# Kernel optimization log

Measured on AMD Instinct MI355X. Metric: run time of the kernel, lower is better.

The kernel has to match this reference:

```python
import jax, jax.numpy as jnp
import numpy as np

B, T_ENC, D = 64, 512, 256
MEL, R = 80, 5
T_DEC = 200
IN = MEL * R  # 400


def _p(key, shape, scale):
    return jax.random.normal(key, shape, dtype=jnp.float32) * scale


def setup_inputs() -> dict:
    key = jax.random.key(0)
    ks = jax.random.split(key, 32)
    s = lambda fan: 1.0 / np.sqrt(fan)
    inp = {
        "enc_out": jax.random.normal(ks[0], (B, T_ENC, D), dtype=jnp.float32),
        "mel_in": jax.random.normal(ks[1], (B, T_DEC, IN), dtype=jnp.float32),
        # prenet: 400 -> 256 -> 128
        "prenet_w1": _p(ks[2], (IN, 256), s(IN)), "prenet_b1": jnp.zeros((256,), jnp.float32),
        "prenet_w2": _p(ks[3], (256, 128), s(256)), "prenet_b2": jnp.zeros((128,), jnp.float32),
        # attention GRUCell: input 128+256=384, hidden 256 (torch gate order r,z,n)
        "att_w_ih": _p(ks[4], (384, 768), s(384)), "att_w_hh": _p(ks[5], (256, 768), s(256)),
        "att_b_ih": jnp.zeros((768,), jnp.float32), "att_b_hh": jnp.zeros((768,), jnp.float32),
        # Bahdanau attention
        "mem_w": _p(ks[6], (D, 256), s(D)),
        "query_w": _p(ks[7], (256, 256), s(256)),
        "att_v": _p(ks[8], (256,), s(256)),
        # project_to_decoder_in: 512 -> 256
        "proj_w": _p(ks[9], (512, 256), s(512)), "proj_b": jnp.zeros((256,), jnp.float32),
        # 2 decoder GRUCells 256->256
        "dec1_w_ih": _p(ks[10], (256, 768), s(256)), "dec1_w_hh": _p(ks[11], (256, 768), s(256)),
        "dec1_b_ih": jnp.zeros((768,), jnp.float32), "dec1_b_hh": jnp.zeros((768,), jnp.float32),
        "dec2_w_ih": _p(ks[12], (256, 768), s(256)), "dec2_w_hh": _p(ks[13], (256, 768), s(256)),
        "dec2_b_ih": jnp.zeros((768,), jnp.float32), "dec2_b_hh": jnp.zeros((768,), jnp.float32),
        # proj_to_mel: 256 -> 400
        "mel_w": _p(ks[14], (256, IN), s(256)), "mel_b": jnp.zeros((IN,), jnp.float32),
    }
    return inp


def _gru(x, h, w_ih, w_hh, b_ih, b_hh):
    gi = x @ w_ih + b_ih
    gh = h @ w_hh + b_hh
    i_r, i_z, i_n = jnp.split(gi, 3, axis=-1)
    h_r, h_z, h_n = jnp.split(gh, 3, axis=-1)
    r = jax.nn.sigmoid(i_r + h_r)
    z = jax.nn.sigmoid(i_z + h_z)
    n = jnp.tanh(i_n + r * h_n)
    return (1.0 - z) * n + z * h


def reference(enc_out, mel_in, prenet_w1, prenet_b1, prenet_w2, prenet_b2,
              att_w_ih, att_w_hh, att_b_ih, att_b_hh, mem_w, query_w, att_v,
              proj_w, proj_b, dec1_w_ih, dec1_w_hh, dec1_b_ih, dec1_b_hh,
              dec2_w_ih, dec2_w_hh, dec2_b_ih, dec2_b_hh, mel_w, mel_b):
    b = enc_out.shape[0]
    # teacher forcing: go frame (zeros) then shifted mel targets
    dec_inputs = jnp.concatenate([jnp.zeros_like(mel_in[:, :1]), mel_in[:, :-1]], axis=1)  # [B,T,400]
    # prenet can be computed for all steps at once (input-only, state-free)
    x = jax.nn.relu(dec_inputs @ prenet_w1 + prenet_b1)
    x = jax.nn.relu(x @ prenet_w2 + prenet_b2)         # [B,T,128]
    xs = jnp.swapaxes(x, 0, 1)                          # [T,B,128]
    proc_mem = enc_out @ mem_w                          # [B,T_enc,256]
    zero = jnp.zeros((b, 256), enc_out.dtype)
    init = (zero, zero, zero, zero)  # att_hidden, context, dec_h1, dec_h2

    def step(carry, xt):
        att_h, ctx, h1, h2 = carry
        att_in = jnp.concatenate([xt, ctx], axis=-1)                 # [B,384]
        att_h = _gru(att_in, att_h, att_w_ih, att_w_hh, att_b_ih, att_b_hh)
        q = att_h @ query_w                                          # [B,256]
        e = jnp.tanh(proc_mem + q[:, None, :]) @ att_v               # [B,T_enc]
        a = jax.nn.softmax(e, axis=-1)
        ctx = jnp.einsum('bt,btd->bd', a, enc_out)                   # [B,256]
        d = jnp.concatenate([att_h, ctx], axis=-1) @ proj_w + proj_b # [B,256]
        h1 = _gru(d, h1, dec1_w_ih, dec1_w_hh, dec1_b_ih, dec1_b_hh)
        d = h1 + d
        h2 = _gru(d, h2, dec2_w_ih, dec2_w_hh, dec2_b_ih, dec2_b_hh)
        d = h2 + d
        out = d @ mel_w + mel_b                                      # [B,400]
        return (att_h, ctx, h1, h2), (out, a)

    _, (outs, aligns) = jax.lax.scan(step, init, xs)
    return jnp.swapaxes(outs, 0, 1), jnp.swapaxes(aligns, 0, 1)
```

## Files before the change

kernel.cpp:

```cpp
#include <hip/hip_runtime.h>
#include <hip/hip_bf16.h>

#define BB   64
#define TT   200
#define TE   512
#define DD   256
#define HH   256
#define GG   768
#define INW  400
#define PN1  256
#define PN2  128

__device__ __forceinline__ float bf2f(unsigned short u) {
    return __uint_as_float(((unsigned)u) << 16);
}
__device__ __forceinline__ float fast_tanh(float x) {
    x = fminf(fmaxf(x, -15.f), 15.f);
    float e = __expf(2.f * x);
    return __fdividef(e - 1.f, e + 1.f);
}
__device__ __forceinline__ float sigm(float x) {
    return __fdividef(1.f, 1.f + __expf(-x));
}

#define FMA4(acc, w4, x0, x1, x2, x3) \
    acc = fmaf(x0, w4.x, acc); acc = fmaf(x1, w4.y, acc); \
    acc = fmaf(x2, w4.z, acc); acc = fmaf(x3, w4.w, acc)

template<int AMODE, int SMODE, bool RELU, bool BIAS>
__global__ __launch_bounds__(256) void gemm_k(
    const float* __restrict__ A, const float* __restrict__ Bm,
    const float* __restrict__ bias, void* __restrict__ Cp,
    int M, int N, int K, int lda, int ldb)
{
    __shared__ __align__(16) float As[16][68];
    __shared__ __align__(16) float Bs[16][68];
    int tid = threadIdx.x;
    int m0 = blockIdx.y * 64, n0 = blockIdx.x * 64;
    int tx = tid & 15, ty = tid >> 4;
    float acc[4][4] = {};
    for (int k0 = 0; k0 < K; k0 += 16) {
        {
            int row = tid >> 2, kq = tid & 3;
            int gr = m0 + row;
            float4 a4;
            if (AMODE == 0) {
                a4 = *(const float4*)(A + (size_t)gr * lda + k0 + kq * 4);
            } else {
                int bb = gr / TT, t = gr % TT;
                if (t == 0) a4 = make_float4(0.f, 0.f, 0.f, 0.f);
                else a4 = *(const float4*)(A + ((size_t)bb * TT + (t - 1)) * INW + k0 + kq * 4);
            }
            As[kq * 4 + 0][row] = a4.x; As[kq * 4 + 1][row] = a4.y;
            As[kq * 4 + 2][row] = a4.z; As[kq * 4 + 3][row] = a4.w;
            int kk = tid >> 4, nq = tid & 15;
            int gc = n0 + nq * 4;
            float4 b4;
            if (gc + 3 < N) {
                b4 = *(const float4*)(Bm + (size_t)(k0 + kk) * ldb + gc);
            } else {
                b4.x = (gc + 0 < N) ? Bm[(size_t)(k0 + kk) * ldb + gc + 0] : 0.f;
                b4.y = (gc + 1 < N) ? Bm[(size_t)(k0 + kk) * ldb + gc + 1] : 0.f;
                b4.z = (gc + 2 < N) ? Bm[(size_t)(k0 + kk) * ldb + gc + 2] : 0.f;
                b4.w = (gc + 3 < N) ? Bm[(size_t)(k0 + kk) * ldb + gc + 3] : 0.f;
            }
            *(float4*)&Bs[kk][nq * 4] = b4;
        }
        __syncthreads();
#pragma unroll
        for (int kk = 0; kk < 16; ++kk) {
            float4 av = *(const float4*)&As[kk][ty * 4];
            float4 bv = *(const float4*)&Bs[kk][tx * 4];
            acc[0][0] = fmaf(av.x, bv.x, acc[0][0]); acc[0][1] = fmaf(av.x, bv.y, acc[0][1]);
            acc[0][2] = fmaf(av.x, bv.z, acc[0][2]); acc[0][3] = fmaf(av.x, bv.w, acc[0][3]);
            acc[1][0] = fmaf(av.y, bv.x, acc[1][0]); acc[1][1] = fmaf(av.y, bv.y, acc[1][1]);
            acc[1][2] = fmaf(av.y, bv.z, acc[1][2]); acc[1][3] = fmaf(av.y, bv.w, acc[1][3]);
            acc[2][0] = fmaf(av.z, bv.x, acc[2][0]); acc[2][1] = fmaf(av.z, bv.y, acc[2][1]);
            acc[2][2] = fmaf(av.z, bv.z, acc[2][2]); acc[2][3] = fmaf(av.z, bv.w, acc[2][3]);
            acc[3][0] = fmaf(av.w, bv.x, acc[3][0]); acc[3][1] = fmaf(av.w, bv.y, acc[3][1]);
            acc[3][2] = fmaf(av.w, bv.z, acc[3][2]); acc[3][3] = fmaf(av.w, bv.w, acc[3][3]);
        }
        __syncthreads();
    }
#pragma unroll
    for (int i = 0; i < 4; ++i) {
#pragma unroll
        for (int j = 0; j < 4; ++j) {
            int r = m0 + ty * 4 + i, c = n0 + tx * 4 + j;
            if (c >= N) continue;
            float v = acc[i][j];
            if (BIAS) v += bias[c];
            if (RELU) v = fmaxf(v, 0.f);
            if (SMODE == 0) ((float*)Cp)[(size_t)r * N + c] = v;
            else if (SMODE == 1) ((float*)Cp)[((size_t)(r % TT) * GG + c) * 64 + (r / TT)] = v;
            else if (SMODE == 2) ((__hip_bfloat16*)Cp)[(size_t)r * N + c] = __float2bfloat16(v);
            else ((float*)Cp)[(size_t)c * M + r] = v;
        }
    }
}

template<bool BF16>
__global__ __launch_bounds__(256) void trans_k(const float* __restrict__ in, int IR, int IC,
                                               int rowoff, void* __restrict__ out)
{
    int idx = blockIdx.x * 256 + threadIdx.x;
    if (idx >= IR * IC) return;
    int c = idx / IR, r = idx % IR;
    float v = in[(size_t)(r + rowoff) * IC + c];
    if (BF16) ((__hip_bfloat16*)out)[idx] = __float2bfloat16(v);
    else ((float*)out)[idx] = v;
}

__global__ __launch_bounds__(256) void tobf16_k(const float* __restrict__ in,
                                                __hip_bfloat16* __restrict__ out, size_t n)
{
    for (size_t i = (size_t)blockIdx.x * 256 + threadIdx.x; i < n; i += (size_t)gridDim.x * 256)
        out[i] = __float2bfloat16(in[i]);
}

__global__ __launch_bounds__(256) void bfuse_k(const float* __restrict__ bih,
                                               const float* __restrict__ projb,
                                               const float* __restrict__ W, int N,
                                               float* __restrict__ out)
{
    int c = blockIdx.x * 256 + threadIdx.x;
    if (c >= N) return;
    float s = bih[c];
    for (int j = 0; j < 256; ++j) s = fmaf(projb[j], W[(size_t)j * N + c], s);
    out[c] = s;
}

__global__ __launch_bounds__(256) void s1_attgru(
    const float* __restrict__ xgi_t, const float* __restrict__ ctxT,
    const float* __restrict__ hT, float* __restrict__ hTn,
    const float* __restrict__ WihcT, const float* __restrict__ WhhT,
    const float* __restrict__ bhh)
{
    int tid = threadIdx.x;
    int b = tid & 63, q = tid >> 6;
    int ul = q >> 1, role = q & 1;
    int u = blockIdx.x * 2 + ul;
    const float* st = (role == 0) ? ctxT : hT;
    const float* W  = (role == 0) ? WihcT : WhhT;
    const float* w0 = W + (size_t)u * 256;
    const float* w1 = W + (size_t)(256 + u) * 256;
    const float* w2 = W + (size_t)(512 + u) * 256;
    float s0 = 0.f, s1 = 0.f, s2 = 0.f;
    for (int j = 0; j < 256; j += 4) {
        float4 a0 = *(const float4*)(w0 + j);
        float4 a1 = *(const float4*)(w1 + j);
        float4 a2 = *(const float4*)(w2 + j);
        float x0 = st[(j + 0) * 64 + b], x1 = st[(j + 1) * 64 + b];
        float x2 = st[(j + 2) * 64 + b], x3 = st[(j + 3) * 64 + b];
        FMA4(s0, a0, x0, x1, x2, x3);
        FMA4(s1, a1, x0, x1, x2, x3);
        FMA4(s2, a2, x0, x1, x2, x3);
    }
    __shared__ float xch[2][3][64];
    if (role == 1) {
        xch[ul][0][b] = s0 + bhh[u];
        xch[ul][1][b] = s1 + bhh[256 + u];
        xch[ul][2][b] = s2 + bhh[512 + u];
    }
    __syncthreads();
    if (role == 0) {
        float ir = s0 + xgi_t[(size_t)u * 64 + b];
        float iz = s1 + xgi_t[(size_t)(256 + u) * 64 + b];
        float in_ = s2 + xgi_t[(size_t)(512 + u) * 64 + b];
        float hr = xch[ul][0][b], hz = xch[ul][1][b], hn = xch[ul][2][b];
        float r = sigm(ir + hr), z = sigm(iz + hz);
        float n = fast_tanh(in_ + r * hn);
        float hp = hT[(size_t)u * 64 + b];
        hTn[(size_t)u * 64 + b] = (1.f - z) * n + z * hp;
    }
}

__global__ __launch_bounds__(256) void s2a_scores(
    const float* __restrict__ hTn, const __hip_bfloat16* __restrict__ WqT,
    const __hip_bfloat16* __restrict__ pmB, const float* __restrict__ v,
    float* __restrict__ evals)
{
    int b = blockIdx.x >> 2, quarter = blockIdx.x & 3;
    int tid = threadIdx.x;
    __shared__ float hsh[256], qsh[256], vsh[256];
    hsh[tid] = hTn[(size_t)tid * 64 + b];
    vsh[tid] = v[tid];
    __syncthreads();
    {
        const unsigned short* wr = (const unsigned short*)(WqT + (size_t)tid * 256);
        float acc = 0.f;
        for (int j = 0; j < 256; j += 4) {
            ushort4 w4 = *(const ushort4*)(wr + j);
            acc = fmaf(hsh[j + 0], bf2f(w4.x), acc);
            acc = fmaf(hsh[j + 1], bf2f(w4.y), acc);
            acc = fmaf(hsh[j + 2], bf2f(w4.z), acc);
            acc = fmaf(hsh[j + 3], bf2f(w4.w), acc);
        }
        qsh[tid] = acc;
    }
    __syncthreads();
    int jl = tid >> 1, half = tid & 1;
    int j = quarter * 128 + jl;
    const unsigned short* pr =
        (const unsigned short*)(pmB + ((size_t)b * TE + j) * 256 + half * 128);
    int kb = half * 128;
    float acc = 0.f;
    for (int k = 0; k < 128; k += 4) {
        ushort4 m4 = *(const ushort4*)(pr + k);
        acc = fmaf(vsh[kb + k + 0], fast_tanh(bf2f(m4.x) + qsh[kb + k + 0]), acc);
        acc = fmaf(vsh[kb + k + 1], fast_tanh(bf2f(m4.y) + qsh[kb + k + 1]), acc);
        acc = fmaf(vsh[kb + k + 2], fast_tanh(bf2f(m4.z) + qsh[kb + k + 2]), acc);
        acc = fmaf(vsh[kb + k + 3], fast_tanh(bf2f(m4.w) + qsh[kb + k + 3]), acc);
    }
    acc += __shfl_xor(acc, 1);
    if (half == 0) evals[(size_t)b * TE + j] = acc;
}

__global__ __launch_bounds__(256) void s2b_ctx(
    const float* __restrict__ evals, const __hip_bfloat16* __restrict__ encB,
    float* __restrict__ ctxTn, float* __restrict__ aligns, int t)
{
    int b = blockIdx.x, tid = threadIdx.x;
    float e0 = evals[(size_t)b * TE + tid];
    float e1 = evals[(size_t)b * TE + 256 + tid];
    float m = fmaxf(e0, e1);
    for (int o = 32; o; o >>= 1) m = fmaxf(m, __shfl_xor(m, o));
    __shared__ float red[4], red2[4], ash[512];
    if ((tid & 63) == 0) red[tid >> 6] = m;
    __syncthreads();
    m = fmaxf(fmaxf(red[0], red[1]), fmaxf(red[2], red[3]));
    float p0 = __expf(e0 - m), p1 = __expf(e1 - m);
    float s = p0 + p1;
    for (int o = 32; o; o >>= 1) s += __shfl_xor(s, o);
    if ((tid & 63) == 0) red2[tid >> 6] = s;
    __syncthreads();
    s = red2[0] + red2[1] + red2[2] + red2[3];
    float inv = __fdividef(1.f, s);
    float a0 = p0 * inv, a1 = p1 * inv;
    ash[tid] = a0; ash[256 + tid] = a1;
    size_t ao = ((size_t)b * TT + t) * TE;
    aligns[ao + tid] = a0;
    aligns[ao + 256 + tid] = a1;
    __syncthreads();
    const unsigned short* er = (const unsigned short*)(encB + (size_t)b * TE * 256) + tid;
    float acc = 0.f;
    for (int j = 0; j < 512; j += 2) {
        acc = fmaf(ash[j + 0], bf2f(er[(size_t)(j + 0) * 256]), acc);
        acc = fmaf(ash[j + 1], bf2f(er[(size_t)(j + 1) * 256]), acc);
    }
    ctxTn[(size_t)tid * 64 + b] = acc;
}

__global__ __launch_bounds__(256) void s4_dec1(
    const float* __restrict__ hTn, const float* __restrict__ ctxTn,
    const float* __restrict__ h1T, float* __restrict__ h1Tn,
    const float* __restrict__ F1T, const float* __restrict__ Whh1T,
    const float* __restrict__ bf1, const float* __restrict__ bhh1)
{
    int tid = threadIdx.x;
    int b = tid & 63, q = tid >> 6;
    int ul = q >> 1, role = q & 1;
    int u = blockIdx.x * 2 + ul;
    float s0 = 0.f, s1 = 0.f, s2 = 0.f;
    __shared__ float xch[2][3][64];
    if (role == 0) {
        const float* w0 = F1T + (size_t)u * 512;
        const float* w1 = F1T + (size_t)(256 + u) * 512;
        const float* w2 = F1T + (size_t)(512 + u) * 512;
        for (int j = 0; j < 256; j += 4) {
            float4 a0 = *(const float4*)(w0 + j);
            float4 a1 = *(const float4*)(w1 + j);
            float4 a2 = *(const float4*)(w2 + j);
            float x0 = hTn[(j + 0) * 64 + b], x1 = hTn[(j + 1) * 64 + b];
            float x2 = hTn[(j + 2) * 64 + b], x3 = hTn[(j + 3) * 64 + b];
            FMA4(s0, a0, x0, x1, x2, x3);
            FMA4(s1, a1, x0, x1, x2, x3);
            FMA4(s2, a2, x0, x1, x2, x3);
        }
        for (int j = 0; j < 256; j += 4) {
            float4 a0 = *(const float4*)(w0 + 256 + j);
            float4 a1 = *(const float4*)(w1 + 256 + j);
            float4 a2 = *(const float4*)(w2 + 256 + j);
            float x0 = ctxTn[(j + 0) * 64 + b], x1 = ctxTn[(j + 1) * 64 + b];
            float x2 = ctxTn[(j + 2) * 64 + b], x3 = ctxTn[(j + 3) * 64 + b];
            FMA4(s0, a0, x0, x1, x2, x3);
            FMA4(s1, a1, x0, x1, x2, x3);
            FMA4(s2, a2, x0, x1, x2, x3);
        }
        s0 += bf1[u]; s1 += bf1[256 + u]; s2 += bf1[512 + u];
    } else {
        const float* w0 = Whh1T + (size_t)u * 256;
        const float* w1 = Whh1T + (size_t)(256 + u) * 256;
        const float* w2 = Whh1T + (size_t)(512 + u) * 256;
        for (int j = 0; j < 256; j += 4) {
            float4 a0 = *(const float4*)(w0 + j);
            float4 a1 = *(const float4*)(w1 + j);
            float4 a2 = *(const float4*)(w2 + j);
            float x0 = h1T[(j + 0) * 64 + b], x1 = h1T[(j + 1) * 64 + b];
            float x2 = h1T[(j + 2) * 64 + b], x3 = h1T[(j + 3) * 64 + b];
            FMA4(s0, a0, x0, x1, x2, x3);
            FMA4(s1, a1, x0, x1, x2, x3);
            FMA4(s2, a2, x0, x1, x2, x3);
        }
        xch[ul][0][b] = s0 + bhh1[u];
        xch[ul][1][b] = s1 + bhh1[256 + u];
        xch[ul][2][b] = s2 + bhh1[512 + u];
    }
    __syncthreads();
    if (role == 0) {
        float hr = xch[ul][0][b], hz = xch[ul][1][b], hn = xch[ul][2][b];
        float r = sigm(s0 + hr), z = sigm(s1 + hz);
        float n = fast_tanh(s2 + r * hn);
        float hp = h1T[(size_t)u * 64 + b];
        h1Tn[(size_t)u * 64 + b] = (1.f - z) * n + z * hp;
    }
}

__global__ __launch_bounds__(256) void s5_dec2(
    const float* __restrict__ hTn, const float* __restrict__ ctxTn,
    const float* __restrict__ h1Tn, const float* __restrict__ h2T,
    float* __restrict__ h2Tn,
    const float* __restrict__ F2T, const float* __restrict__ Wih2T,
    const float* __restrict__ Whh2T,
    const float* __restrict__ b2c, const float* __restrict__ bhh2)
{
    int tid = threadIdx.x;
    int b = tid & 63, q = tid >> 6;
    int ul = q >> 1, role = q & 1;
    int u = blockIdx.x * 2 + ul;
    __shared__ float xch[2][6][64];
    float s0 = 0.f, s1 = 0.f, s2 = 0.f;
    if (role == 0) {
        const float* w0 = F2T + (size_t)u * 512;
        const float* w1 = F2T + (size_t)(256 + u) * 512;
        const float* w2 = F2T + (size_t)(512 + u) * 512;
        for (int j = 0; j < 256; j += 4) {
            float4 a0 = *(const float4*)(w0 + j);
            float4 a1 = *(const float4*)(w1 + j);
            float4 a2 = *(const float4*)(w2 + j);
            float x0 = hTn[(j + 0) * 64 + b], x1 = hTn[(j + 1) * 64 + b];
            float x2 = hTn[(j + 2) * 64 + b], x3 = hTn[(j + 3) * 64 + b];
            FMA4(s0, a0, x0, x1, x2, x3);
            FMA4(s1, a1, x0, x1, x2, x3);
            FMA4(s2, a2, x0, x1, x2, x3);
        }
        for (int j = 0; j < 256; j += 4) {
            float4 a0 = *(const float4*)(w0 + 256 + j);
            float4 a1 = *(const float4*)(w1 + 256 + j);
            float4 a2 = *(const float4*)(w2 + 256 + j);
            float x0 = ctxTn[(j + 0) * 64 + b], x1 = ctxTn[(j + 1) * 64 + b];
            float x2 = ctxTn[(j + 2) * 64 + b], x3 = ctxTn[(j + 3) * 64 + b];
            FMA4(s0, a0, x0, x1, x2, x3);
            FMA4(s1, a1, x0, x1, x2, x3);
            FMA4(s2, a2, x0, x1, x2, x3);
        }
        s0 += b2c[u]; s1 += b2c[256 + u]; s2 += b2c[512 + u];
    } else {
        const float* g0 = Whh2T + (size_t)u * 256;
        const float* g1 = Whh2T + (size_t)(256 + u) * 256;
        const float* g2 = Whh2T + (size_t)(512 + u) * 256;
        const float* x0p = Wih2T + (size_t)u * 256;
        const float* x1p = Wih2T + (size_t)(256 + u) * 256;
        const float* x2p = Wih2T + (size_t)(512 + u) * 256;
        float t0 = 0.f, t1 = 0.f, t2 = 0.f;
        for (int j = 0; j < 256; j += 4) {
            float4 a0 = *(const float4*)(g0 + j);
            float4 a1 = *(const float4*)(g1 + j);
            float4 a2 = *(const float4*)(g2 + j);
            float x0 = h2T[(j + 0) * 64 + b], x1 = h2T[(j + 1) * 64 + b];
            float x2 = h2T[(j + 2) * 64 + b], x3 = h2T[(j + 3) * 64 + b];
            FMA4(s0, a0, x0, x1, x2, x3);
            FMA4(s1, a1, x0, x1, x2, x3);
            FMA4(s2, a2, x0, x1, x2, x3);
        }
        for (int j = 0; j < 256; j += 4) {
            float4 a0 = *(const float4*)(x0p + j);
            float4 a1 = *(const float4*)(x1p + j);
            float4 a2 = *(const float4*)(x2p + j);
            float x0 = h1Tn[(j + 0) * 64 + b], x1 = h1Tn[(j + 1) * 64 + b];
            float x2 = h1Tn[(j + 2) * 64 + b], x3 = h1Tn[(j + 3) * 64 + b];
            FMA4(t0, a0, x0, x1, x2, x3);
            FMA4(t1, a1, x0, x1, x2, x3);
            FMA4(t2, a2, x0, x1, x2, x3);
        }
        xch[ul][0][b] = s0 + bhh2[u];
        xch[ul][1][b] = s1 + bhh2[256 + u];
        xch[ul][2][b] = s2 + bhh2[512 + u];
        xch[ul][3][b] = t0; xch[ul][4][b] = t1; xch[ul][5][b] = t2;
    }
    __syncthreads();
    if (role == 0) {
        float hr = xch[ul][0][b], hz = xch[ul][1][b], hn = xch[ul][2][b];
        float ir = s0 + xch[ul][3][b], iz = s1 + xch[ul][4][b], in_ = s2 + xch[ul][5][b];
        float r = sigm(ir + hr), z = sigm(iz + hz);
        float n = fast_tanh(in_ + r * hn);
        float hp = h2T[(size_t)u * 64 + b];
        h2Tn[(size_t)u * 64 + b] = (1.f - z) * n + z * hp;
    }
}

__global__ __launch_bounds__(256) void s6_mel(
    const float* __restrict__ h1Tn, const float* __restrict__ h2Tn,
    const float* __restrict__ hTn, const float* __restrict__ ctxTn,
    const float* __restrict__ melT, const float* __restrict__ FMT,
    const float* __restrict__ bmc, float* __restrict__ outs, int t)
{
    int tid = threadIdx.x;
    int b = tid & 63, q = tid >> 6;
    int c = blockIdx.x * 4 + q;
    const float* w = melT + (size_t)c * 256;
    const float* f = FMT + (size_t)c * 512;
    float acc = bmc[c];
    for (int j = 0; j < 256; j += 4) {
        float4 w4 = *(const float4*)(w + j);
        float x0 = h1Tn[(j + 0) * 64 + b] + h2Tn[(j + 0) * 64 + b];
        float x1 = h1Tn[(j + 1) * 64 + b] + h2Tn[(j + 1) * 64 + b];
        float x2 = h1Tn[(j + 2) * 64 + b] + h2Tn[(j + 2) * 64 + b];
        float x3 = h1Tn[(j + 3) * 64 + b] + h2Tn[(j + 3) * 64 + b];
        FMA4(acc, w4, x0, x1, x2, x3);
    }
    for (int j = 0; j < 256; j += 4) {
        float4 f4 = *(const float4*)(f + j);
        float x0 = hTn[(j + 0) * 64 + b], x1 = hTn[(j + 1) * 64 + b];
        float x2 = hTn[(j + 2) * 64 + b], x3 = hTn[(j + 3) * 64 + b];
        FMA4(acc, f4, x0, x1, x2, x3);
    }
    for (int j = 0; j < 256; j += 4) {
        float4 f4 = *(const float4*)(f + 256 + j);
        float x0 = ctxTn[(j + 0) * 64 + b], x1 = ctxTn[(j + 1) * 64 + b];
        float x2 = ctxTn[(j + 2) * 64 + b], x3 = ctxTn[(j + 3) * 64 + b];
        FMA4(acc, f4, x0, x1, x2, x3);
    }
    outs[((size_t)b * TT + t) * INW + c] = acc;
}

extern "C" void kernel_launch(void* const* d_in, const int* in_sizes, int n_in,
                              void* d_out, int out_size, void* d_ws, size_t ws_size,
                              hipStream_t stream) {
    const float* enc     = (const float*)d_in[0];
    const float* mel     = (const float*)d_in[1];
    const float* pw1     = (const float*)d_in[2];
    const float* pb1     = (const float*)d_in[3];
    const float* pw2     = (const float*)d_in[4];
    const float* pb2     = (const float*)d_in[5];
    const float* att_wih = (const float*)d_in[6];
    const float* att_whh = (const float*)d_in[7];
    const float* att_bih = (const float*)d_in[8];
    const float* att_bhh = (const float*)d_in[9];
    const float* mem_w   = (const float*)d_in[10];
    const float* query_w = (const float*)d_in[11];
    const float* att_v   = (const float*)d_in[12];
    const float* proj_w  = (const float*)d_in[13];
    const float* proj_b  = (const float*)d_in[14];
    const float* d1_wih  = (const float*)d_in[15];
    const float* d1_whh  = (const float*)d_in[16];
    const float* d1_bih  = (const float*)d_in[17];
    const float* d1_bhh  = (const float*)d_in[18];
    const float* d2_wih  = (const float*)d_in[19];
    const float* d2_whh  = (const float*)d_in[20];
    const float* d2_bih  = (const float*)d_in[21];
    const float* d2_bhh  = (const float*)d_in[22];
    const float* mel_w   = (const float*)d_in[23];
    const float* mel_b   = (const float*)d_in[24];

    float* outs = (float*)d_out;
    float* aligns = outs + (size_t)BB * TT * INW;

    char* p = (char*)d_ws;
    auto take = [&](size_t bytes) -> char* {
        char* r = p;
        p += (bytes + 255) & ~(size_t)255;
        return r;
    };
    const size_t SB = (size_t)HH * BB;
    float* states = (float*)take(8 * SB * 4);
    float* attH = states;
    float* ctxS = states + 2 * SB;
    float* h1S  = states + 4 * SB;
    float* h2S  = states + 6 * SB;
    float* xgi = (float*)take((size_t)TT * GG * BB * 4);
    float* X1  = (float*)take((size_t)BB * TT * PN1 * 4);
    float* X2  = (float*)take((size_t)BB * TT * PN2 * 4);
    __hip_bfloat16* pmB  = (__hip_bfloat16*)take((size_t)BB * TE * DD * 2);
    __hip_bfloat16* encB = (__hip_bfloat16*)take((size_t)BB * TE * DD * 2);
    float* WihcT = (float*)take((size_t)GG * 256 * 4);
    float* WhhT  = (float*)take((size_t)GG * 256 * 4);
    float* Whh1T = (float*)take((size_t)GG * 256 * 4);
    float* Whh2T = (float*)take((size_t)GG * 256 * 4);
    float* Wih2T = (float*)take((size_t)GG * 256 * 4);
    float* melT  = (float*)take((size_t)INW * 256 * 4);
    float* F1T   = (float*)take((size_t)GG * 512 * 4);
    float* F2T   = (float*)take((size_t)GG * 512 * 4);
    float* FMT   = (float*)take((size_t)INW * 512 * 4);
    __hip_bfloat16* WqT = (__hip_bfloat16*)take((size_t)256 * 256 * 2);
    float* bf1 = (float*)take(GG * 4);
    float* b2c = (float*)take(GG * 4);
    float* bmc = (float*)take(INW * 4);
    float* evals = (float*)take((size_t)BB * TE * 4);

    hipMemsetAsync(states, 0, 8 * SB * 4, stream);

    trans_k<false><<<(256 * GG + 255) / 256, 256, 0, stream>>>(att_wih, 256, GG, 128, WihcT);
    trans_k<false><<<(256 * GG + 255) / 256, 256, 0, stream>>>(att_whh, 256, GG, 0, WhhT);
    trans_k<false><<<(256 * GG + 255) / 256, 256, 0, stream>>>(d1_whh, 256, GG, 0, Whh1T);
    trans_k<false><<<(256 * GG + 255) / 256, 256, 0, stream>>>(d2_whh, 256, GG, 0, Whh2T);
    trans_k<false><<<(256 * GG + 255) / 256, 256, 0, stream>>>(d2_wih, 256, GG, 0, Wih2T);
    trans_k<false><<<(256 * INW + 255) / 256, 256, 0, stream>>>(mel_w, 256, INW, 0, melT);
    trans_k<true><<<(256 * 256 + 255) / 256, 256, 0, stream>>>(query_w, 256, 256, 0, WqT);
    tobf16_k<<<8192, 256, 0, stream>>>(enc, encB, (size_t)BB * TE * DD);
    bfuse_k<<<3, 256, 0, stream>>>(d1_bih, proj_b, d1_wih, GG, bf1);
    bfuse_k<<<3, 256, 0, stream>>>(d2_bih, proj_b, d2_wih, GG, b2c);
    bfuse_k<<<2, 256, 0, stream>>>(mel_b, proj_b, mel_w, INW, bmc);

    gemm_k<1, 0, true, true><<<dim3(PN1 / 64, BB * TT / 64), 256, 0, stream>>>(
        mel, pw1, pb1, X1, BB * TT, PN1, INW, INW, PN1);
    gemm_k<0, 0, true, true><<<dim3(PN2 / 64, BB * TT / 64), 256, 0, stream>>>(
        X1, pw2, pb2, X2, BB * TT, PN2, PN1, PN1, PN2);
    gemm_k<0, 1, false, true><<<dim3(GG / 64, BB * TT / 64), 256, 0, stream>>>(
        X2, att_wih, att_bih, xgi, BB * TT, GG, PN2, PN2, GG);
    gemm_k<0, 2, false, false><<<dim3(DD / 64, BB * TE / 64), 256, 0, stream>>>(
        enc, mem_w, nullptr, pmB, BB * TE, DD, DD, DD, DD);
    gemm_k<0, 3, false, false><<<dim3(GG / 64, 512 / 64), 256, 0, stream>>>(
        proj_w, d1_wih, nullptr, F1T, 512, GG, 256, 256, GG);
    gemm_k<0, 3, false, false><<<dim3(GG / 64, 512 / 64), 256, 0, stream>>>(
        proj_w, d2_wih, nullptr, F2T, 512, GG, 256, 256, GG);
    gemm_k<0, 3, false, false><<<dim3((INW + 63) / 64, 512 / 64), 256, 0, stream>>>(
        proj_w, mel_w, nullptr, FMT, 512, INW, 256, 256, INW);

    for (int t = 0; t < TT; ++t) {
        int cur = t & 1, nxt = cur ^ 1;
        float* hC = attH + cur * SB;  float* hN = attH + nxt * SB;
        float* cC = ctxS + cur * SB;  float* cN = ctxS + nxt * SB;
        float* h1C = h1S + cur * SB;  float* h1N = h1S + nxt * SB;
        float* h2C = h2S + cur * SB;  float* h2N = h2S + nxt * SB;

        s1_attgru<<<128, 256, 0, stream>>>(xgi + (size_t)t * GG * BB, cC, hC, hN,
                                           WihcT, WhhT, att_bhh);
        s2a_scores<<<256, 256, 0, stream>>>(hN, WqT, pmB, att_v, evals);
        s2b_ctx<<<64, 256, 0, stream>>>(evals, encB, cN, aligns, t);
        s4_dec1<<<128, 256, 0, stream>>>(hN, cN, h1C, h1N, F1T, Whh1T, bf1, d1_bhh);
        s5_dec2<<<128, 256, 0, stream>>>(hN, cN, h1N, h2C, h2N, F2T, Wih2T, Whh2T,
                                         b2c, d2_bhh);
        s6_mel<<<100, 256, 0, stream>>>(h1N, h2N, hN, cN, melT, FMT, bmc, outs, t);
    }
}
```

Measured before the change: 21.45 ms.

## Replace per-step kernel launches with persistent megakernel using grid barriers

The six per-timestep kernels are merged into one persistent kernel of 128 blocks that runs all 200 decoder steps, separated by atomic-counter grid barriers. This removes roughly 1200 kernel launches and their gaps. The change also folds the tanh scaling into mem_w and v so attention uses raw exp2/rcp, transposes the encoder output to bf16 for the context reduction, and writes mel outputs transposed and fixes them up afterwards. The risks are that the spin barrier deadlocks if all 128 blocks are not co-resident, and that each barrier adds latency.

```diff
diff --git a/kernel.cpp b/kernel.cpp
--- a/kernel.cpp
+++ b/kernel.cpp
@@ -10,17 +10,26 @@
 #define INW  400
 #define PN1  256
 #define PN2  128
-
-__device__ __forceinline__ float bf2f(unsigned short u) {
-    return __uint_as_float(((unsigned)u) << 16);
-}
-__device__ __forceinline__ float fast_tanh(float x) {
-    x = fminf(fmaxf(x, -15.f), 15.f);
-    float e = __expf(2.f * x);
-    return __fdividef(e - 1.f, e + 1.f);
-}
-__device__ __forceinline__ float sigm(float x) {
-    return __fdividef(1.f, 1.f + __expf(-x));
+#define GBLK 128
+#define CSC  2.8853900817779268f
+#define L2E  1.4426950408889634f
+
+typedef unsigned short ushortT;
+
+__device__ __forceinline__ float blo(unsigned u) { return __uint_as_float(u << 16); }
+__device__ __forceinline__ float bhi(unsigned u) { return __uint_as_float(u & 0xffff0000u); }
+
+__device__ __forceinline__ float sigmf_(float x) {
+    return __builtin_amdgcn_rcpf(1.f + __builtin_amdgcn_exp2f(-L2E * x));
+}
+__device__ __forceinline__ float tanhf_(float x) {
+    return 1.f - 2.f * __builtin_amdgcn_rcpf(__builtin_amdgcn_exp2f(CSC * x) + 1.f);
+}
+__device__ __forceinline__ float gru_h(float ir, float iz, float in_, float hr, float hz,
+                                       float hn, float hp) {
+    float r = sigmf_(ir + hr), z = sigmf_(iz + hz);
+    float n = tanhf_(in_ + r * hn);
+    return (1.f - z) * n + z * hp;
 }
 
 #define FMA4(acc, w4, x0, x1, x2, x3) \
@@ -111,11 +120,18 @@
     else ((float*)out)[idx] = v;
 }
 
-__global__ __launch_bounds__(256) void tobf16_k(const float* __restrict__ in,
-                                                __hip_bfloat16* __restrict__ out, size_t n)
-{
-    for (size_t i = (size_t)blockIdx.x * 256 + threadIdx.x; i < n; i += (size_t)gridDim.x * 256)
-        out[i] = __float2bfloat16(in[i]);
+__global__ __launch_bounds__(256) void scale_k(const float* __restrict__ in,
+                                               float* __restrict__ out, int n, float s)
+{
+    int i = blockIdx.x * 256 + threadIdx.x;
+    if (i < n) out[i] = in[i] * s;
+}
+
+__global__ __launch_bounds__(256) void vprep_k(const float* __restrict__ v,
+                                               float* __restrict__ vn2)
+{
+    int i = threadIdx.x;
+    if (i < 256) vn2[i] = -2.f * v[i];
 }
 
 __global__ __launch_bounds__(256) void bfuse_k(const float* __restrict__ bih,
@@ -130,308 +146,357 @@
     out[c] = s;
 }
 
-__global__ __launch_bounds__(256) void s1_attgru(
-    const float* __restrict__ xgi_t, const float* __restrict__ ctxT,
-    const float* __restrict__ hT, float* __restrict__ hTn,
-    const float* __restrict__ WihcT, const float* __restrict__ WhhT,
-    const float* __restrict__ bhh)
-{
+__global__ __launch_bounds__(256) void enct_k(const float* __restrict__ enc,
+                                              ushortT* __restrict__ encT)
+{
+    int bid = blockIdx.x;
+    int b = bid >> 6, pt = (bid >> 3) & 7, dt = bid & 7;
+    int p0 = pt * 64, d0 = dt * 32;
+    __shared__ ushortT tl[64][34];
     int tid = threadIdx.x;
-    int b = tid & 63, q = tid >> 6;
-    int ul = q >> 1, role = q & 1;
-    int u = blockIdx.x * 2 + ul;
-    const float* st = (role == 0) ? ctxT : hT;
-    const float* W  = (role == 0) ? WihcT : WhhT;
-    const float* w0 = W + (size_t)u * 256;
-    const float* w1 = W + (size_t)(256 + u) * 256;
-    const float* w2 = W + (size_t)(512 + u) * 256;
-    float s0 = 0.f, s1 = 0.f, s2 = 0.f;
-    for (int j = 0; j < 256; j += 4) {
-        float4 a0 = *(const float4*)(w0 + j);
-        float4 a1 = *(const float4*)(w1 + j);
-        float4 a2 = *(const float4*)(w2 + j);
-        float x0 = st[(j + 0) * 64 + b], x1 = st[(j + 1) * 64 + b];
-        float x2 = st[(j + 2) * 64 + b], x3 = st[(j + 3) * 64 + b];
-        FMA4(s0, a0, x0, x1, x2, x3);
-        FMA4(s1, a1, x0, x1, x2, x3);
-        FMA4(s2, a2, x0, x1, x2, x3);
-    }
-    __shared__ float xch[2][3][64];
-    if (role == 1) {
-        xch[ul][0][b] = s0 + bhh[u];
-        xch[ul][1][b] = s1 + bhh[256 + u];
-        xch[ul][2][b] = s2 + bhh[512 + u];
+    for (int i = tid; i < 64 * 32; i += 256) {
+        int dd = i & 31, pp = i >> 5;
+        float v = enc[((size_t)b * TE + p0 + pp) * DD + d0 + dd];
+        tl[pp][dd] = (ushortT)(__bfloat16_as_ushort(__float2bfloat16(v)));
     }
     __syncthreads();
-    if (role == 0) {
-        float ir = s0 + xgi_t[(size_t)u * 64 + b];
-        float iz = s1 + xgi_t[(size_t)(256 + u) * 64 + b];
-        float in_ = s2 + xgi_t[(size_t)(512 + u) * 64 + b];
-        float hr = xch[ul][0][b], hz = xch[ul][1][b], hn = xch[ul][2][b];
-        float r = sigm(ir + hr), z = sigm(iz + hz);
-        float n = fast_tanh(in_ + r * hn);
-        float hp = hT[(size_t)u * 64 + b];
-        hTn[(size_t)u * 64 + b] = (1.f - z) * n + z * hp;
-    }
-}
-
-__global__ __launch_bounds__(256) void s2a_scores(
-    const float* __restrict__ hTn, const __hip_bfloat16* __restrict__ WqT,
-    const __hip_bfloat16* __restrict__ pmB, const float* __restrict__ v,
-    float* __restrict__ evals)
-{
-    int b = blockIdx.x >> 2, quarter = blockIdx.x & 3;
+    for (int i = tid; i < 32 * 64; i += 256) {
+        int pp = i & 63, dd = i >> 6;
+        encT[((size_t)b * DD + d0 + dd) * TE + p0 + pp] = tl[pp][dd];
+    }
+}
+
+__global__ __launch_bounds__(256) void outtr_k(const float* __restrict__ outsT,
+                                               float* __restrict__ outs)
+{
+    int bid = blockIdx.x;
+    int t = bid / 7, ct = bid % 7;
+    int c0 = ct * 64, cw = (ct == 6) ? (INW - 384) : 64;
+    int cwl = (cw == 64) ? 6 : 4;
+    __shared__ float tile[64][65];
     int tid = threadIdx.x;
-    __shared__ float hsh[256], qsh[256], vsh[256];
-    hsh[tid] = hTn[(size_t)tid * 64 + b];
-    vsh[tid] = v[tid];
+    for (int i = tid; i < cw * 64; i += 256) {
+        int ci = i >> 6, bb = i & 63;
+        tile[ci][bb] = outsT[((size_t)t * INW + c0 + ci) * 64 + bb];
+    }
     __syncthreads();
-    {
-        const unsigned short* wr = (const unsigned short*)(WqT + (size_t)tid * 256);
-        float acc = 0.f;
-        for (int j = 0; j < 256; j += 4) {
-            ushort4 w4 = *(const ushort4*)(wr + j);
-            acc = fmaf(hsh[j + 0], bf2f(w4.x), acc);
-            acc = fmaf(hsh[j + 1], bf2f(w4.y), acc);
-            acc = fmaf(hsh[j + 2], bf2f(w4.z), acc);
-            acc = fmaf(hsh[j + 3], bf2f(w4.w), acc);
-        }
-        qsh[tid] = acc;
-    }
+    for (int i = tid; i < 64 * cw; i += 256) {
+        int bb = i >> cwl, cc = i & (cw - 1);
+        outs[((size_t)bb * TT + t) * INW + c0 + cc] = tile[cc][bb];
+    }
+}
+
+__device__ __forceinline__ void gridbar(unsigned* cnt, unsigned bar) {
     __syncthreads();
-    int jl = tid >> 1, half = tid & 1;
-    int j = quarter * 128 + jl;
-    const unsigned short* pr =
-        (const unsigned short*)(pmB + ((size_t)b * TE + j) * 256 + half * 128);
-    int kb = half * 128;
-    float acc = 0.f;
-    for (int k = 0; k < 128; k += 4) {
-        ushort4 m4 = *(const ushort4*)(pr + k);
-        acc = fmaf(vsh[kb + k + 0], fast_tanh(bf2f(m4.x) + qsh[kb + k + 0]), acc);
-        acc = fmaf(vsh[kb + k + 1], fast_tanh(bf2f(m4.y) + qsh[kb + k + 1]), acc);
-        acc = fmaf(vsh[kb + k + 2], fast_tanh(bf2f(m4.z) + qsh[kb + k + 2]), acc);
-        acc = fmaf(vsh[kb + k + 3], fast_tanh(bf2f(m4.w) + qsh[kb + k + 3]), acc);
-    }
-    acc += __shfl_xor(acc, 1);
-    if (half == 0) evals[(size_t)b * TE + j] = acc;
-}
-
-__global__ __launch_bounds__(256) void s2b_ctx(
-    const float* __restrict__ evals, const __hip_bfloat16* __restrict__ encB,
-    float* __restrict__ ctxTn, float* __restrict__ aligns, int t)
-{
-    int b = blockIdx.x, tid = threadIdx.x;
-    float e0 = evals[(size_t)b * TE + tid];
-    float e1 = evals[(size_t)b * TE + 256 + tid];
-    float m = fmaxf(e0, e1);
-    for (int o = 32; o; o >>= 1) m = fmaxf(m, __shfl_xor(m, o));
-    __shared__ float red[4], red2[4], ash[512];
-    if ((tid & 63) == 0) red[tid >> 6] = m;
+    if (threadIdx.x == 0) {
+        __threadfence();
+        __hip_atomic_fetch_add(cnt, 1u, __ATOMIC_RELAXED, __HIP_MEMORY_SCOPE_AGENT);
+        unsigned target = bar * (unsigned)GBLK;
+        while (__hip_atomic_load(cnt, __ATOMIC_RELAXED, __HIP_MEMORY_SCOPE_AGENT) < target) {
+            __builtin_amdgcn_s_sleep(1);
+        }
+        __threadfence();
+    }
     __syncthreads();
-    m = fmaxf(fmaxf(red[0], red[1]), fmaxf(red[2], red[3]));
-    float p0 = __expf(e0 - m), p1 = __expf(e1 - m);
-    float s = p0 + p1;
-    for (int o = 32; o; o >>= 1) s += __shfl_xor(s, o);
-    if ((tid & 63) == 0) red2[tid >> 6] = s;
-    __syncthreads();
-    s = red2[0] + red2[1] + red2[2] + red2[3];
-    float inv = __fdividef(1.f, s);
-    float a0 = p0 * inv, a1 = p1 * inv;
-    ash[tid] = a0; ash[256 + tid] = a1;
-    size_t ao = ((size_t)b * TT + t) * TE;
-    aligns[ao + tid] = a0;
-    aligns[ao + 256 + tid] = a1;
-    __syncthreads();
-    const unsigned short* er = (const unsigned short*)(encB + (size_t)b * TE * 256) + tid;
-    float acc = 0.f;
-    for (int j = 0; j < 512; j += 2) {
-        acc = fmaf(ash[j + 0], bf2f(er[(size_t)(j + 0) * 256]), acc);
-        acc = fmaf(ash[j + 1], bf2f(er[(size_t)(j + 1) * 256]), acc);
-    }
-    ctxTn[(size_t)tid * 64 + b] = acc;
-}
-
-__global__ __launch_bounds__(256) void s4_dec1(
-    const float* __restrict__ hTn, const float* __restrict__ ctxTn,
-    const float* __restrict__ h1T, float* __restrict__ h1Tn,
+}
+
+__device__ __forceinline__ float tpair(unsigned u32, int d, const float* qk,
+                                       const float* vn2, float acc) {
+    float xa = blo(u32) + qk[d];
+    float xb = bhi(u32) + qk[d + 1];
+    float ra = __builtin_amdgcn_rcpf(__builtin_amdgcn_exp2f(xa) + 1.f);
+    float rb = __builtin_amdgcn_rcpf(__builtin_amdgcn_exp2f(xb) + 1.f);
+    acc = fmaf(vn2[d], ra, acc);
+    return fmaf(vn2[d + 1], rb, acc);
+}
+
+__global__ __launch_bounds__(512, 2) void mega_k(
+    const float* __restrict__ xgi, const float* __restrict__ WihcT,
+    const float* __restrict__ WhhT, const float* __restrict__ att_bhh,
     const float* __restrict__ F1T, const float* __restrict__ Whh1T,
-    const float* __restrict__ bf1, const float* __restrict__ bhh1)
-{
-    int tid = threadIdx.x;
-    int b = tid & 63, q = tid >> 6;
-    int ul = q >> 1, role = q & 1;
-    int u = blockIdx.x * 2 + ul;
-    float s0 = 0.f, s1 = 0.f, s2 = 0.f;
-    __shared__ float xch[2][3][64];
-    if (role == 0) {
-        const float* w0 = F1T + (size_t)u * 512;
-        const float* w1 = F1T + (size_t)(256 + u) * 512;
-        const float* w2 = F1T + (size_t)(512 + u) * 512;
-        for (int j = 0; j < 256; j += 4) {
-            float4 a0 = *(const float4*)(w0 + j);
-            float4 a1 = *(const float4*)(w1 + j);
-            float4 a2 = *(const float4*)(w2 + j);
-            float x0 = hTn[(j + 0) * 64 + b], x1 = hTn[(j + 1) * 64 + b];
-            float x2 = hTn[(j + 2) * 64 + b], x3 = hTn[(j + 3) * 64 + b];
-            FMA4(s0, a0, x0, x1, x2, x3);
-            FMA4(s1, a1, x0, x1, x2, x3);
-            FMA4(s2, a2, x0, x1, x2, x3);
-        }
-        for (int j = 0; j < 256; j += 4) {
-            float4 a0 = *(const float4*)(w0 + 256 + j);
-            float4 a1 = *(const float4*)(w1 + 256 + j);
-            float4 a2 = *(const float4*)(w2 + 256 + j);
-            float x0 = ctxTn[(j + 0) * 64 + b], x1 = ctxTn[(j + 1) * 64 + b];
-            float x2 = ctxTn[(j + 2) * 64 + b], x3 = ctxTn[(j + 3) * 64 + b];
-            FMA4(s0, a0, x0, x1, x2, x3);
-            FMA4(s1, a1, x0, x1, x2, x3);
-            FMA4(s2, a2, x0, x1, x2, x3);
-        }
-        s0 += bf1[u]; s1 += bf1[256 + u]; s2 += bf1[512 + u];
-    } else {
-        const float* w0 = Whh1T + (size_t)u * 256;
-        const float* w1 = Whh1T + (size_t)(256 + u) * 256;
-        const float* w2 = Whh1T + (size_t)(512 + u) * 256;
-        for (int j = 0; j < 256; j += 4) {
-            float4 a0 = *(const float4*)(w0 + j);
-            float4 a1 = *(const float4*)(w1 + j);
-            float4 a2 = *(const float4*)(w2 + j);
-            float x0 = h1T[(j + 0) * 64 + b], x1 = h1T[(j + 1) * 64 + b];
-            float x2 = h1T[(j + 2) * 64 + b], x3 = h1T[(j + 3) * 64 + b];
-            FMA4(s0, a0, x0, x1, x2, x3);
-            FMA4(s1, a1, x0, x1, x2, x3);
-            FMA4(s2, a2, x0, x1, x2, x3);
-        }
-        xch[ul][0][b] = s0 + bhh1[u];
-        xch[ul][1][b] = s1 + bhh1[256 + u];
-        xch[ul][2][b] = s2 + bhh1[512 + u];
-    }
-    __syncthreads();
-    if (role == 0) {
-        float hr = xch[ul][0][b], hz = xch[ul][1][b], hn = xch[ul][2][b];
-        float r = sigm(s0 + hr), z = sigm(s1 + hz);
-        float n = fast_tanh(s2 + r * hn);
-        float hp = h1T[(size_t)u * 64 + b];
-        h1Tn[(size_t)u * 64 + b] = (1.f - z) * n + z * hp;
-    }
-}
-
-__global__ __launch_bounds__(256) void s5_dec2(
-    const float* __restrict__ hTn, const float* __restrict__ ctxTn,
-    const float* __restrict__ h1Tn, const float* __restrict__ h2T,
-    float* __restrict__ h2Tn,
+    const float* __restrict__ bf1, const float* __restrict__ d1_bhh,
     const float* __restrict__ F2T, const float* __restrict__ Wih2T,
-    const float* __restrict__ Whh2T,
-    const float* __restrict__ b2c, const float* __restrict__ bhh2)
-{
-    int tid = threadIdx.x;
-    int b = tid & 63, q = tid >> 6;
-    int ul = q >> 1, role = q & 1;
-    int u = blockIdx.x * 2 + ul;
-    __shared__ float xch[2][6][64];
-    float s0 = 0.f, s1 = 0.f, s2 = 0.f;
-    if (role == 0) {
-        const float* w0 = F2T + (size_t)u * 512;
-        const float* w1 = F2T + (size_t)(256 + u) * 512;
-        const float* w2 = F2T + (size_t)(512 + u) * 512;
-        for (int j = 0; j < 256; j += 4) {
-            float4 a0 = *(const float4*)(w0 + j);
-            float4 a1 = *(const float4*)(w1 + j);
-            float4 a2 = *(const float4*)(w2 + j);
-            float x0 = hTn[(j + 0) * 64 + b], x1 = hTn[(j + 1) * 64 + b];
-            float x2 = hTn[(j + 2) * 64 + b], x3 = hTn[(j + 3) * 64 + b];
-            FMA4(s0, a0, x0, x1, x2, x3);
-            FMA4(s1, a1, x0, x1, x2, x3);
-            FMA4(s2, a2, x0, x1, x2, x3);
-        }
-        for (int j = 0; j < 256; j += 4) {
-            float4 a0 = *(const float4*)(w0 + 256 + j);
-            float4 a1 = *(const float4*)(w1 + 256 + j);
-            float4 a2 = *(const float4*)(w2 + 256 + j);
-            float x0 = ctxTn[(j + 0) * 64 + b], x1 = ctxTn[(j + 1) * 64 + b];
-            float x2 = ctxTn[(j + 2) * 64 + b], x3 = ctxTn[(j + 3) * 64 + b];
-            FMA4(s0, a0, x0, x1, x2, x3);
-            FMA4(s1, a1, x0, x1, x2, x3);
-            FMA4(s2, a2, x0, x1, x2, x3);
-        }
-        s0 += b2c[u]; s1 += b2c[256 + u]; s2 += b2c[512 + u];
-    } else {
-        const float* g0 = Whh2T + (size_t)u * 256;
-        const float* g1 = Whh2T + (size_t)(256 + u) * 256;
-        const float* g2 = Whh2T + (size_t)(512 + u) * 256;
-        const float* x0p = Wih2T + (size_t)u * 256;
-        const float* x1p = Wih2T + (size_t)(256 + u) * 256;
-        const float* x2p = Wih2T + (size_t)(512 + u) * 256;
-        float t0 = 0.f, t1 = 0.f, t2 = 0.f;
-        for (int j = 0; j < 256; j += 4) {
-            float4 a0 = *(const float4*)(g0 + j);
-            float4 a1 = *(const float4*)(g1 + j);
-            float4 a2 = *(const float4*)(g2 + j);
-            float x0 = h2T[(j + 0) * 64 + b], x1 = h2T[(j + 1) * 64 + b];
-            float x2 = h2T[(j + 2) * 64 + b], x3 = h2T[(j + 3) * 64 + b];
-            FMA4(s0, a0, x0, x1, x2, x3);
-            FMA4(s1, a1, x0, x1, x2, x3);
-            FMA4(s2, a2, x0, x1, x2, x3);
-        }
-        for (int j = 0; j < 256; j += 4) {
-            float4 a0 = *(const float4*)(x0p + j);
-            float4 a1 = *(const float4*)(x1p + j);
-            float4 a2 = *(const float4*)(x2p + j);
-            float x0 = h1Tn[(j + 0) * 64 + b], x1 = h1Tn[(j + 1) * 64 + b];
-            float x2 = h1Tn[(j + 2) * 64 + b], x3 = h1Tn[(j + 3) * 64 + b];
-            FMA4(t0, a0, x0, x1, x2, x3);
-            FMA4(t1, a1, x0, x1, x2, x3);
-            FMA4(t2, a2, x0, x1, x2, x3);
-        }
-        xch[ul][0][b] = s0 + bhh2[u];
-        xch[ul][1][b] = s1 + bhh2[256 + u];
-        xch[ul][2][b] = s2 + bhh2[512 + u];
-        xch[ul][3][b] = t0; xch[ul][4][b] = t1; xch[ul][5][b] = t2;
-    }
-    __syncthreads();
-    if (role == 0) {
-        float hr = xch[ul][0][b], hz = xch[ul][1][b], hn = xch[ul][2][b];
-        float ir = s0 + xch[ul][3][b], iz = s1 + xch[ul][4][b], in_ = s2 + xch[ul][5][b];
-        float r = sigm(ir + hr), z = sigm(iz + hz);
-        float n = fast_tanh(in_ + r * hn);
-        float hp = h2T[(size_t)u * 64 + b];
-        h2Tn[(size_t)u * 64 + b] = (1.f - z) * n + z * hp;
-    }
-}
-
-__global__ __launch_bounds__(256) void s6_mel(
-    const float* __restrict__ h1Tn, const float* __restrict__ h2Tn,
-    const float* __restrict__ hTn, const float* __restrict__ ctxTn,
+    const float* __restrict__ Whh2T, const float* __restrict__ b2c,
+    const float* __restrict__ d2_bhh,
     const float* __restrict__ melT, const float* __restrict__ FMT,
-    const float* __restrict__ bmc, float* __restrict__ outs, int t)
-{
-    int tid = threadIdx.x;
-    int b = tid & 63, q = tid >> 6;
-    int c = blockIdx.x * 4 + q;
-    const float* w = melT + (size_t)c * 256;
-    const float* f = FMT + (size_t)c * 512;
-    float acc = bmc[c];
-    for (int j = 0; j < 256; j += 4) {
-        float4 w4 = *(const float4*)(w + j);
-        float x0 = h1Tn[(j + 0) * 64 + b] + h2Tn[(j + 0) * 64 + b];
-        float x1 = h1Tn[(j + 1) * 64 + b] + h2Tn[(j + 1) * 64 + b];
-        float x2 = h1Tn[(j + 2) * 64 + b] + h2Tn[(j + 2) * 64 + b];
-        float x3 = h1Tn[(j + 3) * 64 + b] + h2Tn[(j + 3) * 64 + b];
-        FMA4(acc, w4, x0, x1, x2, x3);
-    }
-    for (int j = 0; j < 256; j += 4) {
-        float4 f4 = *(const float4*)(f + j);
-        float x0 = hTn[(j + 0) * 64 + b], x1 = hTn[(j + 1) * 64 + b];
-        float x2 = hTn[(j + 2) * 64 + b], x3 = hTn[(j + 3) * 64 + b];
-        FMA4(acc, f4, x0, x1, x2, x3);
-    }
-    for (int j = 0; j < 256; j += 4) {
-        float4 f4 = *(const float4*)(f + 256 + j);
-        float x0 = ctxTn[(j + 0) * 64 + b], x1 = ctxTn[(j + 1) * 64 + b];
-        float x2 = ctxTn[(j + 2) * 64 + b], x3 = ctxTn[(j + 3) * 64 + b];
-        FMA4(acc, f4, x0, x1, x2, x3);
-    }
-    outs[((size_t)b * TT + t) * INW + c] = acc;
+    const float* __restrict__ bmc,
+    const ushortT* __restrict__ WqT, const ushortT* __restrict__ pmB,
+    const ushortT* __restrict__ encT, const float* __restrict__ vn2g,
+    float* __restrict__ states, float* __restrict__ outsT,
+    float* __restrict__ aligns, unsigned* __restrict__ cnt)
+{
+    const int tid = threadIdx.x, bid = blockIdx.x;
+    const int lane = tid & 63, wq = tid >> 6;
+    __shared__ __align__(16) float smem[2600];
+    float* part = smem;
+    unsigned bar = 0;
+    const size_t SB = (size_t)HH * BB;
+    float* attH = states;
+    float* ctxS = states + 2 * SB;
+    float* h1S  = states + 4 * SB;
+    float* h2S  = states + 6 * SB;
+
+#define PPART(q, g) part[((q) * 3 + (g)) * 64 + lane]
+
+    for (int t = 0; t < TT; ++t) {
+        const int cur = t & 1, nxt = cur ^ 1;
+        const float* hC  = attH + cur * SB;  float* hN  = attH + nxt * SB;
+        const float* cC  = ctxS + cur * SB;  float* cN  = ctxS + nxt * SB;
+        const float* h1C = h1S + cur * SB;   float* h1N = h1S + nxt * SB;
+        const float* h2C = h2S + cur * SB;   float* h2N = h2S + nxt * SB;
+        const float* xgi_t = xgi + (size_t)t * (GG * 64);
+
+        {
+            int ul = wq & 1, kh = (wq >> 1) & 1, role = wq >> 2;
+            int u = bid * 2 + ul;
+            const float* W  = role ? WhhT : WihcT;
+            const float* st = (role ? hC : cC) + kh * 128 * 64 + lane;
+            const float* w0 = W + ((size_t)u) * 256 + kh * 128;
+            const float* w1 = W + ((size_t)(256 + u)) * 256 + kh * 128;
+            const float* w2 = W + ((size_t)(512 + u)) * 256 + kh * 128;
+            float s0 = 0.f, s1 = 0.f, s2 = 0.f;
+            for (int j = 0; j < 128; j += 4) {
+                float4 a0 = *(const float4*)(w0 + j);
+                float4 a1 = *(const float4*)(w1 + j);
+                float4 a2 = *(const float4*)(w2 + j);
+                float x0 = st[(j + 0) * 64], x1 = st[(j + 1) * 64];
+                float x2 = st[(j + 2) * 64], x3 = st[(j + 3) * 64];
+                FMA4(s0, a0, x0, x1, x2, x3);
+                FMA4(s1, a1, x0, x1, x2, x3);
+                FMA4(s2, a2, x0, x1, x2, x3);
+            }
+            PPART(wq, 0) = s0; PPART(wq, 1) = s1; PPART(wq, 2) = s2;
+            __syncthreads();
+            if (wq < 2) {
+                int uu = bid * 2 + wq;
+                float ir  = PPART(wq, 0) + PPART(wq + 2, 0) + xgi_t[(size_t)uu * 64 + lane];
+                float iz  = PPART(wq, 1) + PPART(wq + 2, 1) + xgi_t[(size_t)(256 + uu) * 64 + lane];
+                float in_ = PPART(wq, 2) + PPART(wq + 2, 2) + xgi_t[(size_t)(512 + uu) * 64 + lane];
+                float hr  = PPART(wq + 4, 0) + PPART(wq + 6, 0) + att_bhh[uu];
+                float hz  = PPART(wq + 4, 1) + PPART(wq + 6, 1) + att_bhh[256 + uu];
+                float hn  = PPART(wq + 4, 2) + PPART(wq + 6, 2) + att_bhh[512 + uu];
+                float hp  = hC[(size_t)uu * 64 + lane];
+                hN[(size_t)uu * 64 + lane] = gru_h(ir, iz, in_, hr, hz, hn, hp);
+            }
+        }
+        gridbar(cnt, ++bar);
+
+        if (bid < BB) {
+            const int b = bid;
+            float* hsh   = smem;
+            float* qk    = smem + 256;
+            float* vn2   = smem + 512;
+            float* ash   = smem + 768;
+            float* red   = smem + 1280;
+            float* cpart = smem + 1312;
+            if (tid < 256) { hsh[tid] = hN[(size_t)tid * 64 + b]; vn2[tid] = vn2g[tid]; }
+            __syncthreads();
+            if (tid < 256) {
+                const ushortT* wr = WqT + (size_t)tid * 256;
+                float acc = 0.f;
+                for (int k = 0; k < 256; k += 8) {
+                    uint4 w = *(const uint4*)(wr + k);
+                    acc = fmaf(hsh[k + 0], blo(w.x), acc); acc = fmaf(hsh[k + 1], bhi(w.x), acc);
+                    acc = fmaf(hsh[k + 2], blo(w.y), acc); acc = fmaf(hsh[k + 3], bhi(w.y), acc);
+                    acc = fmaf(hsh[k + 4], blo(w.z), acc); acc = fmaf(hsh[k + 5], bhi(w.z), acc);
+                    acc = fmaf(hsh[k + 6], blo(w.w), acc); acc = fmaf(hsh[k + 7], bhi(w.w), acc);
+                }
+                qk[tid] = acc * CSC;
+            }
+            __syncthreads();
+            const ushortT* pr = pmB + ((size_t)b * TE + tid) * 256;
+            float e = 0.f;
+            for (int d = 0; d < 256; d += 8) {
+                uint4 w = *(const uint4*)(pr + d);
+                e = tpair(w.x, d + 0, qk, vn2, e);
+                e = tpair(w.y, d + 2, qk, vn2, e);
+                e = tpair(w.z, d + 4, qk, vn2, e);
+                e = tpair(w.w, d + 6, qk, vn2, e);
+            }
+            float m = e;
+            for (int o = 32; o; o >>= 1) m = fmaxf(m, __shfl_xor(m, o));
+            if (lane == 0) red[wq] = m;
+            __syncthreads();
+            m = red[0];
+            for (int i = 1; i < 8; ++i) m = fmaxf(m, red[i]);
+            float pe = __builtin_amdgcn_exp2f((e - m) * L2E);
+            float ssum = pe;
+            for (int o = 32; o; o >>= 1) ssum += __shfl_xor(ssum, o);
+            __syncthreads();
+            if (lane == 0) red[wq] = ssum;
+            __syncthreads();
+            ssum = red[0] + red[1] + red[2] + red[3] + red[4] + red[5] + red[6] + red[7];
+            float a = pe * __builtin_amdgcn_rcpf(ssum);
+            ash[tid] = a;
+            aligns[((size_t)b * TT + t) * TE + tid] = a;
+            __syncthreads();
+            int d = tid & 255, ph = tid >> 8;
+            const ushortT* er = encT + ((size_t)(b * DD + d)) * TE + ph * 256;
+            const float* ap = ash + ph * 256;
+            float acc = 0.f;
+            for (int p = 0; p < 256; p += 8) {
+                uint4 w = *(const uint4*)(er + p);
+                acc = fmaf(ap[p + 0], blo(w.x), acc); acc = fmaf(ap[p + 1], bhi(w.x), acc);
+                acc = fmaf(ap[p + 2], blo(w.y), acc); acc = fmaf(ap[p + 3], bhi(w.y), acc);
+                acc = fmaf(ap[p + 4], blo(w.z), acc); acc = fmaf(ap[p + 5], bhi(w.z), acc);
+                acc = fmaf(ap[p + 6], blo(w.w), acc); acc = fmaf(ap[p + 7], bhi(w.w), acc);
+            }
+            cpart[ph * 256 + d] = acc;
+            __syncthreads();
+            if (tid < 256) cN[(size_t)tid * 64 + b] = cpart[tid] + cpart[256 + tid];
+        }
+        gridbar(cnt, ++bar);
+
+        {
+            int ul = wq & 1, sub = wq >> 1;
+            int u = bid * 2 + ul;
+            float s0 = 0.f, s1 = 0.f, s2 = 0.f;
+            if (sub < 2) {
+                const float* st = (sub ? cN : hN) + lane;
+                const float* w0 = F1T + ((size_t)u) * 512 + sub * 256;
+                const float* w1 = F1T + ((size_t)(256 + u)) * 512 + sub * 256;
+                const float* w2 = F1T + ((size_t)(512 + u)) * 512 + sub * 256;
+                for (int j = 0; j < 256; j += 4) {
+                    float4 a0 = *(const float4*)(w0 + j);
+                    float4 a1 = *(const float4*)(w1 + j);
+                    float4 a2 = *(const float4*)(w2 + j);
+                    float x0 = st[(j + 0) * 64], x1 = st[(j + 1) * 64];
+                    float x2 = st[(j + 2) * 64], x3 = st[(j + 3) * 64];
+                    FMA4(s0, a0, x0, x1, x2, x3);
+                    FMA4(s1, a1, x0, x1, x2, x3);
+                    FMA4(s2, a2, x0, x1, x2, x3);
+                }
+            } else {
+                int kh = sub - 2;
+                const float* st = h1C + kh * 128 * 64 + lane;
+                const float* w0 = Whh1T + ((size_t)u) * 256 + kh * 128;
+                const float* w1 = Whh1T + ((size_t)(256 + u)) * 256 + kh * 128;
+                const float* w2 = Whh1T + ((size_t)(512 + u)) * 256 + kh * 128;
+                for (int j = 0; j < 128; j += 4) {
+                    float4 a0 = *(const float4*)(w0 + j);
+                    float4 a1 = *(const float4*)(w1 + j);
+                    float4 a2 = *(const float4*)(w2 + j);
+                    float x0 = st[(j + 0) * 64], x1 = st[(j + 1) * 64];
+                    float x2 = st[(j + 2) * 64], x3 = st[(j + 3) * 64];
+                    FMA4(s0, a0, x0, x1, x2, x3);
+                    FMA4(s1, a1, x0, x1, x2, x3);
+                    FMA4(s2, a2, x0, x1, x2, x3);
+                }
+            }
+            PPART(wq, 0) = s0; PPART(wq, 1) = s1; PPART(wq, 2) = s2;
+            __syncthreads();
+            if (wq < 2) {
+                int uu = bid * 2 + wq;
+                float ir  = PPART(wq, 0) + PPART(wq + 2, 0) + bf1[uu];
+                float iz  = PPART(wq, 1) + PPART(wq + 2, 1) + bf1[256 + uu];
+                float in_ = PPART(wq, 2) + PPART(wq + 2, 2) + bf1[512 + uu];
+                float hr  = PPART(wq + 4, 0) + PPART(wq + 6, 0) + d1_bhh[uu];
+                float hz  = PPART(wq + 4, 1) + PPART(wq + 6, 1) + d1_bhh[256 + uu];
+                float hn  = PPART(wq + 4, 2) + PPART(wq + 6, 2) + d1_bhh[512 + uu];
+                float hp  = h1C[(size_t)uu * 64 + lane];
+                h1N[(size_t)uu * 64 + lane] = gru_h(ir, iz, in_, hr, hz, hn, hp);
+            }
+        }
+        gridbar(cnt, ++bar);
+
+        {
+            int ul = wq & 1, sub = wq >> 1;
+            int u = bid * 2 + ul;
+            float s0 = 0.f, s1 = 0.f, s2 = 0.f;
+            const float* st; const float* w0; const float* w1; const float* w2;
+            if (sub == 0) {
+                st = hN + lane;
+                w0 = F2T + ((size_t)u) * 512;
+                w1 = F2T + ((size_t)(256 + u)) * 512;
+                w2 = F2T + ((size_t)(512 + u)) * 512;
+            } else if (sub == 1) {
+                st = cN + lane;
+                w0 = F2T + ((size_t)u) * 512 + 256;
+                w1 = F2T + ((size_t)(256 + u)) * 512 + 256;
+                w2 = F2T + ((size_t)(512 + u)) * 512 + 256;
+            } else if (sub == 2) {
+                st = h1N + lane;
+                w0 = Wih2T + ((size_t)u) * 256;
+                w1 = Wih2T + ((size_t)(256 + u)) * 256;
+                w2 = Wih2T + ((size_t)(512 + u)) * 256;
+            } else {
+                st = h2C + lane;
+                w0 = Whh2T + ((size_t)u) * 256;
+                w1 = Whh2T + ((size_t)(256 + u)) * 256;
+                w2 = Whh2T + ((size_t)(512 + u)) * 256;
+            }
+            for (int j = 0; j < 256; j += 4) {
+                float4 a0 = *(const float4*)(w0 + j);
+                float4 a1 = *(const float4*)(w1 + j);
+                float4 a2 = *(const float4*)(w2 + j);
+                float x0 = st[(j + 0) * 64], x1 = st[(j + 1) * 64];
+                float x2 = st[(j + 2) * 64], x3 = st[(j + 3) * 64];
+                FMA4(s0, a0, x0, x1, x2, x3);
+                FMA4(s1, a1, x0, x1, x2, x3);
+                FMA4(s2, a2, x0, x1, x2, x3);
+            }
+            PPART(wq, 0) = s0; PPART(wq, 1) = s1; PPART(wq, 2) = s2;
+            __syncthreads();
+            if (wq < 2) {
+                int uu = bid * 2 + wq;
+                float ir  = PPART(wq, 0) + PPART(wq + 2, 0) + PPART(wq + 4, 0) + b2c[uu];
+                float iz  = PPART(wq, 1) + PPART(wq + 2, 1) + PPART(wq + 4, 1) + b2c[256 + uu];
+                float in_ = PPART(wq, 2) + PPART(wq + 2, 2) + PPART(wq + 4, 2) + b2c[512 + uu];
+                float hr  = PPART(wq + 6, 0) + d2_bhh[uu];
+                float hz  = PPART(wq + 6, 1) + d2_bhh[256 + uu];
+                float hn  = PPART(wq + 6, 2) + d2_bhh[512 + uu];
+                float hp  = h2C[(size_t)uu * 64 + lane];
+                h2N[(size_t)uu * 64 + lane] = gru_h(ir, iz, in_, hr, hz, hn, hp);
+            }
+        }
+        gridbar(cnt, ++bar);
+
+        if (bid < 100) {
+            int colq = wq & 3, kh = wq >> 2;
+            int c = bid * 4 + colq;
+            float acc = 0.f;
+            if (kh == 0) {
+                acc = bmc[c];
+                const float* w = melT + (size_t)c * 256;
+                for (int j = 0; j < 256; j += 4) {
+                    float4 w4 = *(const float4*)(w + j);
+                    float x0 = h1N[(size_t)(j + 0) * 64 + lane] + h2N[(size_t)(j + 0) * 64 + lane];
+                    float x1 = h1N[(size_t)(j + 1) * 64 + lane] + h2N[(size_t)(j + 1) * 64 + lane];
+                    float x2 = h1N[(size_t)(j + 2) * 64 + lane] + h2N[(size_t)(j + 2) * 64 + lane];
+                    float x3 = h1N[(size_t)(j + 3) * 64 + lane] + h2N[(size_t)(j + 3) * 64 + lane];
+                    FMA4(acc, w4, x0, x1, x2, x3);
+                }
+                const float* f = FMT + (size_t)c * 512;
+                for (int j = 0; j < 128; j += 4) {
+                    float4 f4 = *(const float4*)(f + j);
+                    float x0 = hN[(size_t)(j + 0) * 64 + lane], x1 = hN[(size_t)(j + 1) * 64 + lane];
+                    float x2 = hN[(size_t)(j + 2) * 64 + lane], x3 = hN[(size_t)(j + 3) * 64 + lane];
+                    FMA4(acc, f4, x0, x1, x2, x3);
+                }
+            } else {
+                const float* f = FMT + (size_t)c * 512 + 128;
+                for (int j = 0; j < 128; j += 4) {
+                    float4 f4 = *(const float4*)(f + j);
+                    float x0 = hN[(size_t)(128 + j + 0) * 64 + lane], x1 = hN[(size_t)(128 + j + 1) * 64 + lane];
+                    float x2 = hN[(size_t)(128 + j + 2) * 64 + lane], x3 = hN[(size_t)(128 + j + 3) * 64 + lane];
+                    FMA4(acc, f4, x0, x1, x2, x3);
+                }
+                const float* f2 = FMT + (size_t)c * 512 + 256;
+                for (int j = 0; j < 256; j += 4) {
+                    float4 f4 = *(const float4*)(f2 + j);
+                    float x0 = cN[(size_t)(j + 0) * 64 + lane], x1 = cN[(size_t)(j + 1) * 64 + lane];
+                    float x2 = cN[(size_t)(j + 2) * 64 + lane], x3 = cN[(size_t)(j + 3) * 64 + lane];
+                    FMA4(acc, f4, x0, x1, x2, x3);
+                }
+                smem[wq * 64 + lane] = acc;
+            }
+            __syncthreads();
+            if (kh == 0)
+                outsT[((size_t)t * INW + c) * 64 + lane] = acc + smem[(wq + 4) * 64 + lane];
+        }
+        __syncthreads();
+    }
+#undef PPART
 }
 
 extern "C" void kernel_launch(void* const* d_in, const int* in_sizes, int n_in,
@@ -474,15 +539,14 @@
     };
     const size_t SB = (size_t)HH * BB;
     float* states = (float*)take(8 * SB * 4);
-    float* attH = states;
-    float* ctxS = states + 2 * SB;
-    float* h1S  = states + 4 * SB;
-    float* h2S  = states + 6 * SB;
+    unsigned* cnt = (unsigned*)take(256);
+    char* bufA = take((size_t)TT * INW * 64 * 4);
+    float* X1 = (float*)bufA;
+    float* X2 = (float*)(bufA + (size_t)BB * TT * PN1 * 4);
+    float* outsT = (float*)bufA;
     float* xgi = (float*)take((size_t)TT * GG * BB * 4);
-    float* X1  = (float*)take((size_t)BB * TT * PN1 * 4);
-    float* X2  = (float*)take((size_t)BB * TT * PN2 * 4);
     __hip_bfloat16* pmB  = (__hip_bfloat16*)take((size_t)BB * TE * DD * 2);
-    __hip_bfloat16* encB = (__hip_bfloat16*)take((size_t)BB * TE * DD * 2);
+    ushortT* encT = (ushortT*)take((size_t)BB * TE * DD * 2);
     float* WihcT = (float*)take((size_t)GG * 256 * 4);
     float* WhhT  = (float*)take((size_t)GG * 256 * 4);
     float* Whh1T = (float*)take((size_t)GG * 256 * 4);
@@ -493,12 +557,14 @@
     float* F2T   = (float*)take((size_t)GG * 512 * 4);
     float* FMT   = (float*)take((size_t)INW * 512 * 4);
     __hip_bfloat16* WqT = (__hip_bfloat16*)take((size_t)256 * 256 * 2);
+    float* memwS = (float*)take((size_t)DD * 256 * 4);
     float* bf1 = (float*)take(GG * 4);
     float* b2c = (float*)take(GG * 4);
     float* bmc = (float*)take(INW * 4);
-    float* evals = (float*)take((size_t)BB * TE * 4);
-
-    hipMemsetAsync(states, 0, 8 * SB * 4, stream);
+    float* vn2g = (float*)take(256 * 4);
+
+    (void)hipMemsetAsync(states, 0, 8 * SB * 4, stream);
+    (void)hipMemsetAsync(cnt, 0, 256, stream);
 
     trans_k<false><<<(256 * GG + 255) / 256, 256, 0, stream>>>(att_wih, 256, GG, 128, WihcT);
     trans_k<false><<<(256 * GG + 255) / 256, 256, 0, stream>>>(att_whh, 256, GG, 0, WhhT);
@@ -507,7 +573,9 @@
     trans_k<false><<<(256 * GG + 255) / 256, 256, 0, stream>>>(d2_wih, 256, GG, 0, Wih2T);
     trans_k<false><<<(256 * INW + 255) / 256, 256, 0, stream>>>(mel_w, 256, INW, 0, melT);
     trans_k<true><<<(256 * 256 + 255) / 256, 256, 0, stream>>>(query_w, 256, 256, 0, WqT);
-    tobf16_k<<<8192, 256, 0, stream>>>(enc, encB, (size_t)BB * TE * DD);
+    scale_k<<<(DD * 256 + 255) / 256, 256, 0, stream>>>(mem_w, memwS, DD * 256, CSC);
+    vprep_k<<<1, 256, 0, stream>>>(att_v, vn2g);
+    enct_k<<<64 * 64, 256, 0, stream>>>(enc, encT);
     bfuse_k<<<3, 256, 0, stream>>>(d1_bih, proj_b, d1_wih, GG, bf1);
     bfuse_k<<<3, 256, 0, stream>>>(d2_bih, proj_b, d2_wih, GG, b2c);
     bfuse_k<<<2, 256, 0, stream>>>(mel_b, proj_b, mel_w, INW, bmc);
@@ -519,7 +587,7 @@
     gemm_k<0, 1, false, true><<<dim3(GG / 64, BB * TT / 64), 256, 0, stream>>>(
         X2, att_wih, att_bih, xgi, BB * TT, GG, PN2, PN2, GG);
     gemm_k<0, 2, false, false><<<dim3(DD / 64, BB * TE / 64), 256, 0, stream>>>(
-        enc, mem_w, nullptr, pmB, BB * TE, DD, DD, DD, DD);
+        enc, memwS, nullptr, pmB, BB * TE, DD, DD, DD, DD);
     gemm_k<0, 3, false, false><<<dim3(GG / 64, 512 / 64), 256, 0, stream>>>(
         proj_w, d1_wih, nullptr, F1T, 512, GG, 256, 256, GG);
     gemm_k<0, 3, false, false><<<dim3(GG / 64, 512 / 64), 256, 0, stream>>>(
@@ -527,20 +595,13 @@
     gemm_k<0, 3, false, false><<<dim3((INW + 63) / 64, 512 / 64), 256, 0, stream>>>(
         proj_w, mel_w, nullptr, FMT, 512, INW, 256, 256, INW);
 
-    for (int t = 0; t < TT; ++t) {
-        int cur = t & 1, nxt = cur ^ 1;
-        float* hC = attH + cur * SB;  float* hN = attH + nxt * SB;
-        float* cC = ctxS + cur * SB;  float* cN = ctxS + nxt * SB;
-        float* h1C = h1S + cur * SB;  float* h1N = h1S + nxt * SB;
-        float* h2C = h2S + cur * SB;  float* h2N = h2S + nxt * SB;
-
-        s1_attgru<<<128, 256, 0, stream>>>(xgi + (size_t)t * GG * BB, cC, hC, hN,
-                                           WihcT, WhhT, att_bhh);
-        s2a_scores<<<256, 256, 0, stream>>>(hN, WqT, pmB, att_v, evals);
-        s2b_ctx<<<64, 256, 0, stream>>>(evals, encB, cN, aligns, t);
-        s4_dec1<<<128, 256, 0, stream>>>(hN, cN, h1C, h1N, F1T, Whh1T, bf1, d1_bhh);
-        s5_dec2<<<128, 256, 0, stream>>>(hN, cN, h1N, h2C, h2N, F2T, Wih2T, Whh2T,
-                                         b2c, d2_bhh);
-        s6_mel<<<100, 256, 0, stream>>>(h1N, h2N, hN, cN, melT, FMT, bmc, outs, t);
-    }
-}
+    mega_k<<<GBLK, 512, 0, stream>>>(
+        xgi, WihcT, WhhT, att_bhh,
+        F1T, Whh1T, bf1, d1_bhh,
+        F2T, Wih2T, Whh2T, b2c, d2_bhh,
+        melT, FMT, bmc,
+        (const ushortT*)WqT, (const ushortT*)pmB, encT, vn2g,
+        states, outsT, aligns, cnt);
+
+    outtr_k<<<TT * 7, 256, 0, stream>>>(outsT, outs);
+}
```

Measured after the change: 24.71 ms. +15.2%, slower.
